# Kernel tuning notes

Measured on AMD Instinct MI355X. Metric: run time of the kernel, lower is better.

The kernel has to match this reference:

```python
import jax, jax.numpy as jnp
import numpy as np

HIDDEN = 4096
NUM_HEADS = 32
NUM_KV_HEADS = 8
HEAD_DIM = HIDDEN // NUM_HEADS  # 128
Q_SIZE = NUM_HEADS * HEAD_DIM    # 4096
KV_SIZE = NUM_KV_HEADS * HEAD_DIM  # 1024
SCALE = 1.0 / HEAD_DIM  # attention_multiplier=None -> head_dim ** (-1)
ROPE_BASE = 10000.0


def _rope_neox(x, positions):
    # x: [B, S, H, D], positions: [B, S] int
    half = HEAD_DIM // 2
    inv_freq = 1.0 / (ROPE_BASE ** (jnp.arange(0, half, dtype=jnp.float32) / half))
    freqs = positions.astype(jnp.float32)[..., None] * inv_freq  # [B, S, half]
    cos = jnp.cos(freqs)[:, :, None, :]  # [B, S, 1, half]
    sin = jnp.sin(freqs)[:, :, None, :]
    x1, x2 = x[..., :half], x[..., half:]
    return jnp.concatenate([x1 * cos - x2 * sin, x2 * cos + x1 * sin], axis=-1)


def setup_inputs() -> dict:
    key = jax.random.key(0)
    k1, k2, k3 = jax.random.split(key, 3)
    B, S = 2, 2048
    positions = jnp.broadcast_to(jnp.arange(S, dtype=jnp.int32), (B, S))
    hidden_states = jax.random.normal(k1, (B, S, HIDDEN), dtype=jnp.float32) * 0.02
    w_qkv = jax.random.normal(k2, (Q_SIZE + 2 * KV_SIZE, HIDDEN), dtype=jnp.float32) * 0.02
    w_o = jax.random.normal(k3, (HIDDEN, Q_SIZE), dtype=jnp.float32) * 0.02
    return {"positions": positions, "hidden_states": hidden_states, "w_qkv": w_qkv, "w_o": w_o}


def reference(positions, hidden_states, w_qkv, w_o):
    B, S, _ = hidden_states.shape
    # fused QKV projection
    qkv = jnp.einsum('bsh,oh->bso', hidden_states, w_qkv)
    q = qkv[..., :Q_SIZE].reshape(B, S, NUM_HEADS, HEAD_DIM)
    k = qkv[..., Q_SIZE:Q_SIZE + KV_SIZE].reshape(B, S, NUM_KV_HEADS, HEAD_DIM)
    v = qkv[..., Q_SIZE + KV_SIZE:].reshape(B, S, NUM_KV_HEADS, HEAD_DIM)
    # neox-style RoPE on q and k
    q = _rope_neox(q, positions)
    k = _rope_neox(k, positions)
    # GQA: repeat kv heads
    rep = NUM_HEADS // NUM_KV_HEADS
    k = jnp.repeat(k, rep, axis=2)  # [B, S, NUM_HEADS, D]
    v = jnp.repeat(v, rep, axis=2)
    # causal attention
    scores = jnp.einsum('bqhd,bkhd->bhqk', q, k) * SCALE
    causal = jnp.tril(jnp.ones((S, S), dtype=bool))
    scores = jnp.where(causal, scores, jnp.finfo(scores.dtype).min)
    probs = jax.nn.softmax(scores, axis=-1)
    attn = jnp.einsum('bhqk,bkhd->bqhd', probs, v).reshape(B, S, Q_SIZE)
    # output projection
    return jnp.einsum('bsq,hq->bsh', attn, w_o)
```

## Files before the change

### kernel.cpp

```cpp
#include <hip/hip_runtime.h>
#include <hip/hip_bf16.h>
#include <cmath>

typedef __bf16 bf16x8 __attribute__((ext_vector_type(8)));
typedef __bf16 bf16x4 __attribute__((ext_vector_type(4)));
typedef float  f32x4  __attribute__((ext_vector_type(4)));
typedef unsigned int u32;
typedef u32 u32x4 __attribute__((ext_vector_type(4)));

#define AS1 __attribute__((address_space(1)))
#define AS3 __attribute__((address_space(3)))
#define GLDS16(gp, lp) __builtin_amdgcn_global_load_lds((AS1 void*)(gp), (AS3 void*)(lp), 16, 0, 0)

#define B_DIM 2
#define S_LEN 2048
#define HIDDEN 4096
#define NHEADS 32
#define NKV 8
#define HDIM 128
#define QSZ 4096
#define KVSZ 1024
#define QKVSZ 6144
#define GK 4096
#define ATT_SCALE 0.0078125f
#define L2E 1.4426950408889634f

__global__ __launch_bounds__(256) void conv_f32_bf16(const float* __restrict__ in,
                                                     __bf16* __restrict__ out, int n4) {
    int idx = blockIdx.x * 256 + threadIdx.x;
    if (idx < n4) {
        float4 v = ((const float4*)in)[idx];
        bf16x4 o;
        o[0] = (__bf16)v.x; o[1] = (__bf16)v.y; o[2] = (__bf16)v.z; o[3] = (__bf16)v.w;
        ((bf16x4*)out)[idx] = o;
    }
}

__global__ __launch_bounds__(256) void rope_table_kernel(float* __restrict__ ct,
                                                         float* __restrict__ st) {
    int idx = blockIdx.x * 256 + threadIdx.x;
    int p = idx >> 6, i = idx & 63;
    float inv = expf(-(float)i * (9.210340371976184f / 64.0f));
    float freq = (float)p * inv;
    float s, c;
    sincosf(freq, &s, &c);
    ct[idx] = c; st[idx] = s;
}

template<typename OUT>
__global__ __launch_bounds__(512, 2) void gemm256(const __bf16* __restrict__ A,
                                                  const __bf16* __restrict__ B,
                                                  OUT* __restrict__ C,
                                                  int N) {
    __shared__ __bf16 Asm[2 * 16384 + 2 * 16384];
    char* Bbase = (char*)Asm + 65536;

    const int tid = threadIdx.x;
    const int w = tid >> 6, l = tid & 63;
    const int l15 = l & 15, l4 = l >> 4;
    const int wr = w >> 2, wc = w & 3;

    const int nwg = gridDim.x * gridDim.y;
    const int orig = blockIdx.y * gridDim.x + blockIdx.x;
    const int swz = (orig & 7) * (nwg >> 3) + (orig >> 3);
    const int bx = swz % gridDim.x, by = swz / gridDim.x;
    const int m0 = by * 256, n0 = bx * 256;

    const __bf16* Ag = A + (size_t)m0 * GK;
    const __bf16* Bg = B + (size_t)n0 * GK;

#define STAGE_AQ(q, tile) do {                                                  \
        int c_ = (q) * 512 + tid;                                               \
        int r_ = c_ >> 3;                                                       \
        int jg_ = (tid & 7) ^ (r_ & 7);                                         \
        GLDS16(Ag + (size_t)r_ * GK + (tile) * 64 + jg_ * 8,                    \
               (char*)Asm + ((tile) & 1) * 32768 + c_ * 16);                    \
    } while (0)
#define STAGE_BS(s, tile) do {                                                  \
        _Pragma("unroll")                                                       \
        for (int i_ = 0; i_ < 2; ++i_) {                                        \
            int v_ = i_ * 512 + tid;                                            \
            int r_ = (v_ >> 8) * 64 + (s) * 32 + ((v_ >> 3) & 31);              \
            int jg_ = (v_ & 7) ^ (r_ & 7);                                      \
            int c_ = r_ * 8 + (v_ & 7);                                         \
            GLDS16(Bg + (size_t)r_ * GK + (tile) * 64 + jg_ * 8,                \
                   Bbase + ((tile) & 1) * 32768 + c_ * 16);                     \
        }                                                                       \
    } while (0)

#define LOAD_A(DST, MH) do {                                                    \
        _Pragma("unroll")                                                       \
        for (int m2 = 0; m2 < 4; ++m2) {                                        \
            int row = wr * 128 + ((MH) * 4 + m2) * 16 + l15;                    \
            _Pragma("unroll")                                                   \
            for (int kk = 0; kk < 2; ++kk) {                                    \
                int j = (kk * 4 + l4) ^ (row & 7);                              \
                DST[m2][kk] = *(const bf16x8*)(Als + row * 64 + j * 8);         \
            }                                                                   \
        }                                                                       \
    } while (0)
#define LOAD_B(DST, NH) do {                                                    \
        _Pragma("unroll")                                                       \
        for (int n2 = 0; n2 < 2; ++n2) {                                        \
            int row = wc * 64 + ((NH) * 2 + n2) * 16 + l15;                     \
            _Pragma("unroll")                                                   \
            for (int kk = 0; kk < 2; ++kk) {                                    \
                int j = (kk * 4 + l4) ^ (row & 7);                              \
                DST[n2][kk] = *(const bf16x8*)(Bls + row * 64 + j * 8);         \
            }                                                                   \
        }                                                                       \
    } while (0)
#define MFMA_QUAD(AF, BF, MI0, NI0)                                             \
    _Pragma("unroll")                                                           \
    for (int m2 = 0; m2 < 4; ++m2)                                              \
        _Pragma("unroll")                                                       \
        for (int n2 = 0; n2 < 2; ++n2)                                          \
            _Pragma("unroll")                                                   \
            for (int kk = 0; kk < 2; ++kk)                                      \
                acc[(MI0) + m2][(NI0) + n2] =                                   \
                    __builtin_amdgcn_mfma_f32_16x16x32_bf16(                    \
                        AF[m2][kk], BF[n2][kk], acc[(MI0) + m2][(NI0) + n2], 0, 0, 0);
#define PH_SYNC_PRE  do { __builtin_amdgcn_sched_barrier(0);                    \
        __builtin_amdgcn_s_barrier();                                           \
        asm volatile("s_waitcnt lgkmcnt(0)" ::: "memory");                      \
        __builtin_amdgcn_sched_barrier(0); } while (0)
#define PH_SYNC_POST do { __builtin_amdgcn_sched_barrier(0);                    \
        __builtin_amdgcn_s_barrier(); } while (0)

    f32x4 acc[8][4] = {};

    const int T = GK / 64;
    STAGE_AQ(0, 0); STAGE_AQ(1, 0); STAGE_AQ(2, 0); STAGE_AQ(3, 0);
    STAGE_BS(0, 0); STAGE_BS(1, 0);
    STAGE_AQ(0, 1); STAGE_AQ(2, 1); STAGE_BS(0, 1);
    asm volatile("s_waitcnt vmcnt(4)" ::: "memory");
    __builtin_amdgcn_s_barrier();

    for (int t = 0; t < T; ++t) {
        const __bf16* Als = Asm + (t & 1) * 16384;
        const __bf16* Bls = (__bf16*)Bbase + (t & 1) * 16384;
        bf16x8 af0[4][2], af1[4][2], bfr[2][2];
        LOAD_A(af0, 0);
        LOAD_B(bfr, 0);
        if (t + 1 < T) { STAGE_AQ(1, t + 1); STAGE_AQ(3, t + 1); }
        PH_SYNC_PRE;
        __builtin_amdgcn_s_setprio(1);
        MFMA_QUAD(af0, bfr, 0, 0);
        __builtin_amdgcn_s_setprio(0);
        PH_SYNC_POST;
        LOAD_B(bfr, 1);
        if (t + 1 < T) STAGE_BS(1, t + 1);
        PH_SYNC_PRE;
        __builtin_amdgcn_s_setprio(1);
        MFMA_QUAD(af0, bfr, 0, 2);
        __builtin_amdgcn_s_setprio(0);
        PH_SYNC_POST;
        LOAD_A(af1, 1);
        LOAD_B(bfr, 0);
        if (t + 2 < T) { STAGE_AQ(0, t + 2); STAGE_AQ(2, t + 2); }
        PH_SYNC_PRE;
        __builtin_amdgcn_s_setprio(1);
        MFMA_QUAD(af1, bfr, 4, 0);
        __builtin_amdgcn_s_setprio(0);
        PH_SYNC_POST;
        LOAD_B(bfr, 1);
        if (t + 2 < T) STAGE_BS(0, t + 2);
        PH_SYNC_PRE;
        __builtin_amdgcn_s_setprio(1);
        MFMA_QUAD(af1, bfr, 4, 2);
        __builtin_amdgcn_s_setprio(0);
        if (t + 2 < T)      { asm volatile("s_waitcnt vmcnt(4)" ::: "memory"); }
        else if (t + 1 < T) { asm volatile("s_waitcnt vmcnt(0)" ::: "memory"); }
        PH_SYNC_POST;
    }
#undef PH_SYNC_PRE
#undef PH_SYNC_POST
#undef MFMA_QUAD
#undef LOAD_A
#undef LOAD_B
#undef STAGE_AQ
#undef STAGE_BS

#pragma unroll
    for (int mi = 0; mi < 8; ++mi)
#pragma unroll
        for (int ni = 0; ni < 4; ++ni)
#pragma unroll
            for (int r = 0; r < 4; ++r)
                C[(size_t)(m0 + wr * 128 + mi * 16 + l4 * 4 + r) * N
                  + n0 + wc * 64 + ni * 16 + l15] = (OUT)acc[mi][ni][r];
}

__global__ __launch_bounds__(256) void rope_kernel(const __bf16* __restrict__ qkv,
                                                   const int* __restrict__ pos,
                                                   const float* __restrict__ ct,
                                                   const float* __restrict__ st,
                                                   __bf16* __restrict__ Qb,
                                                   __bf16* __restrict__ Kb) {
    const int tid = threadIdx.x;
    const int tok = blockIdx.x;
    const int b = tok >> 11, s = tok & 2047;
    const int p = pos[tok];
    const __bf16* base = qkv + (size_t)tok * QKVSZ;
    const float* cb = ct + (size_t)p * 64;
    const float* sb = st + (size_t)p * 64;
    for (int idx = tid; idx < 2560; idx += 256) {
        int head = idx >> 6, i = idx & 63;
        float c = cb[i], sn = sb[i];
        if (head < 32) {
            float x1 = (float)base[head * HDIM + i];
            float x2 = (float)base[head * HDIM + 64 + i];
            size_t o = ((size_t)(b * 32 + head) * S_LEN + s) * HDIM + i;
            Qb[o]      = (__bf16)((x1 * c - x2 * sn) * ATT_SCALE);
            Qb[o + 64] = (__bf16)((x2 * c + x1 * sn) * ATT_SCALE);
        } else {
            int g = head - 32;
            float x1 = (float)base[QSZ + g * HDIM + i];
            float x2 = (float)base[QSZ + g * HDIM + 64 + i];
            size_t o = ((size_t)(b * 8 + g) * S_LEN + s) * HDIM + i;
            Kb[o]      = (__bf16)(x1 * c - x2 * sn);
            Kb[o + 64] = (__bf16)(x2 * c + x1 * sn);
        }
    }
}

__global__ __launch_bounds__(256) void vtrans_kernel(const __bf16* __restrict__ qkv,
                                                     __bf16* __restrict__ Vt) {
    __shared__ __bf16 T[64][132];
    const int tid = threadIdx.x;
    const int st = blockIdx.x, g = blockIdx.y, b = blockIdx.z;
    const __bf16* src = qkv + ((size_t)(b * S_LEN + st * 64)) * QKVSZ + (QSZ + KVSZ) + g * HDIM;
#pragma unroll
    for (int it = 0; it < 8; ++it) {
        int c = it * 256 + tid;
        int row = c >> 5;
        int c4 = c & 31;
        bf16x4 v = *(const bf16x4*)(src + (size_t)row * QKVSZ + c4 * 4);
        *(bf16x4*)(&T[row][c4 * 4]) = v;
    }
    __syncthreads();
#pragma unroll
    for (int it = 0; it < 8; ++it) {
        int c = it * 256 + tid;
        int d = c >> 4;
        int s4 = (c & 15) * 4;
        bf16x4 o;
        o[0] = T[s4 + 0][d]; o[1] = T[s4 + 1][d]; o[2] = T[s4 + 2][d]; o[3] = T[s4 + 3][d];
        *(bf16x4*)(Vt + ((size_t)(b * 8 + g) * HDIM + d) * S_LEN + st * 64 + s4) = o;
    }
}

__global__ __launch_bounds__(512, 2) void attn_kernel(const __bf16* __restrict__ Q,
                                                      const __bf16* __restrict__ K,
                                                      const __bf16* __restrict__ Vt,
                                                      __bf16* __restrict__ O) {
    const int tid = threadIdx.x;
    const int w = tid >> 6, l = tid & 63;
    const int l15 = l & 15, l4 = l >> 4;
    const int flat = blockIdx.x + (blockIdx.y << 2) + (blockIdx.z << 7);
    const int swz = (flat & 7) * 32 + (flat >> 3);
    const int p = swz & 3;
    const int hb = swz >> 2;
    const int h = hb & 31, b = hb >> 5;
    const int g = h >> 2;

    __shared__ __bf16 Ks[4][64 * 128];
    __shared__ __bf16 Vs[4][128 * 64];

    const __bf16* Kp = K + (size_t)(b * 8 + g) * S_LEN * HDIM;
    const __bf16* Vp = Vt + (size_t)(b * 8 + g) * HDIM * S_LEN;

#define RED16(x, OPINS) do {                                                      \
        u32 ra_ = __builtin_bit_cast(u32, x), rb_;                                \
        asm("v_mov_b32 %0, %1" : "=v"(rb_) : "v"(ra_));                           \
        asm("v_permlane16_swap_b32 %0, %1" : "+v"(ra_), "+v"(rb_));               \
        x = OPINS(__builtin_bit_cast(float, ra_), __builtin_bit_cast(float, rb_));\
    } while (0)
#define RED32(x, OPINS) do {                                                      \
        u32 ra_ = __builtin_bit_cast(u32, x), rb_;                                \
        asm("v_mov_b32 %0, %1" : "=v"(rb_) : "v"(ra_));                           \
        asm("v_permlane32_swap_b32 %0, %1" : "+v"(ra_), "+v"(rb_));               \
        x = OPINS(__builtin_bit_cast(float, ra_), __builtin_bit_cast(float, rb_));\
    } while (0)
#define FADD_(a_, b_) ((a_) + (b_))

#define STAGE(ktile) do {                                                          \
        const int buf_ = (ktile) & 3;                                              \
        const __bf16* kbase = Kp + (size_t)(ktile) * 64 * HDIM;                    \
        _Pragma("unroll")                                                          \
        for (int i_ = 0; i_ < 2; ++i_) {                                           \
            int c_ = i_ * 512 + tid;                \
            int row_ = c_ >> 4, cc_ = (c_ & 15) ^ (row_ & 7);                      \
            GLDS16(kbase + (size_t)row_ * HDIM + cc_ * 8,                          \
                   (char*)Ks[buf_] + c_ * 16);                                     \
        }                                                                          \
        const __bf16* vbase = Vp + (size_t)(ktile) * 64;                           \
        _Pragma("unroll")                                                          \
        for (int i_ = 0; i_ < 2; ++i_) {                                           \
            int c_ = i_ * 512 + tid;                \
            int row_ = c_ >> 3, cc_ = (c_ & 7) ^ (row_ & 7);                       \
            GLDS16(vbase + (size_t)row_ * S_LEN + cc_ * 8,                         \
                   (char*)Vs[buf_] + c_ * 16);                                     \
        }                                                                          \
    } while (0)

    for (int pi = 0; pi < 2; ++pi) {
        const int qt = pi ? (7 - p) : p;
        const int qw0 = qt * 256 + w * 32;
        const __bf16* Qp = Q + ((size_t)((b * 32 + h) * S_LEN + qw0)) * HDIM;

        bf16x8 qf[2][4];
#pragma unroll
        for (int qh = 0; qh < 2; ++qh)
#pragma unroll
            for (int kk = 0; kk < 4; ++kk)
                qf[qh][kk] = *(const bf16x8*)(Qp + (size_t)(qh * 16 + l15) * HDIM + kk * 32 + l4 * 8);

        f32x4 acc[2][8] = {};
        float m[2]    = {-1e30f, -1e30f};
        float lsum[2] = {0.f, 0.f};

        const int nkt = 4 * qt + 4;
        if (pi) { asm volatile("s_waitcnt vmcnt(0)" ::: "memory"); }
        STAGE(0);
        STAGE(1);
        STAGE(2);

        for (int kt = 0; kt < nkt; ++kt) {
            if (kt + 3 < nkt) STAGE(kt + 3);
            {
                int rem = nkt - 1 - kt;
                if (rem >= 3)      { asm volatile("s_waitcnt vmcnt(12)" ::: "memory"); }
                else if (rem == 2) { asm volatile("s_waitcnt vmcnt(8)"  ::: "memory"); }
                else if (rem == 1) { asm volatile("s_waitcnt vmcnt(4)"  ::: "memory"); }
                else               { asm volatile("s_waitcnt vmcnt(0)"  ::: "memory"); }
            }
            __builtin_amdgcn_sched_barrier(0);
            __builtin_amdgcn_s_barrier();
            __builtin_amdgcn_sched_barrier(0);
            const int cur = kt & 3;
            if (kt * 64 <= qw0 + 31) {
                f32x4 sfr[2][4];
                __builtin_amdgcn_s_setprio(1);
#pragma unroll
                for (int fn = 0; fn < 4; ++fn) {
                    f32x4 sa0 = {}, sa1 = {};
#pragma unroll
                    for (int kk = 0; kk < 4; ++kk) {
                        int row = fn * 16 + l15;
                        int cc = (kk * 4 + l4) ^ (l15 & 7);
                        bf16x8 kb = *(const bf16x8*)(Ks[cur] + row * HDIM + cc * 8);
                        sa0 = __builtin_amdgcn_mfma_f32_16x16x32_bf16(kb, qf[0][kk], sa0, 0, 0, 0);
                        sa1 = __builtin_amdgcn_mfma_f32_16x16x32_bf16(kb, qf[1][kk], sa1, 0, 0, 0);
                    }
                    sfr[0][fn] = sa0; sfr[1][fn] = sa1;
                }
                __builtin_amdgcn_s_setprio(0);
                const bool needmask = (kt * 64 + 63 > qw0);
                bf16x8 pb[2][2];
#pragma unroll
                for (int qh = 0; qh < 2; ++qh) {
                    const int qrow = qw0 + qh * 16 + l15;
                    float pmax = -1e30f;
#pragma unroll
                    for (int fn = 0; fn < 4; ++fn)
#pragma unroll
                        for (int r = 0; r < 4; ++r) {
                            float v = sfr[qh][fn][r];
                            if (needmask) {
                                int kcol = kt * 64 + fn * 16 + l4 * 4 + r;
                                if (kcol > qrow) v = -1e30f;
                            }
                            sfr[qh][fn][r] = v;
                            pmax = fmaxf(pmax, v);
                        }
                    RED16(pmax, fmaxf);
                    RED32(pmax, fmaxf);
                    if (!__all(pmax - m[qh] <= 8.0f)) {
                        float mn = fmaxf(m[qh], pmax);
                        float alpha = exp2f((m[qh] - mn) * L2E);
                        m[qh] = mn;
                        lsum[qh] *= alpha;
#pragma unroll
                        for (int n = 0; n < 8; ++n)
#pragma unroll
                            for (int r = 0; r < 4; ++r) acc[qh][n][r] *= alpha;
                    }
                    float rs = 0.f;
                    u32 pk01[4], pk23[4];
#pragma unroll
                    for (int fn = 0; fn < 4; ++fn) {
                        float p0 = exp2f((sfr[qh][fn][0] - m[qh]) * L2E);
                        float p1 = exp2f((sfr[qh][fn][1] - m[qh]) * L2E);
                        float p2 = exp2f((sfr[qh][fn][2] - m[qh]) * L2E);
                        float p3 = exp2f((sfr[qh][fn][3] - m[qh]) * L2E);
                        rs += (p0 + p1) + (p2 + p3);
                        asm("v_cvt_pk_bf16_f32 %0, %1, %2" : "=v"(pk01[fn]) : "v"(p0), "v"(p1));
                        asm("v_cvt_pk_bf16_f32 %0, %1, %2" : "=v"(pk23[fn]) : "v"(p2), "v"(p3));
                    }
                    RED16(rs, FADD_);
                    RED32(rs, FADD_);
                    lsum[qh] += rs;
#pragma unroll
                    for (int kk = 0; kk < 2; ++kk) {
                        u32 w0 = pk01[2 * kk], w2 = pk01[2 * kk + 1];
                        asm("v_permlane32_swap_b32 %0, %1" : "+v"(w0), "+v"(w2));
                        asm("v_permlane16_swap_b32 %0, %1" : "+v"(w0), "+v"(w2));
                        u32 w1 = pk23[2 * kk], w3 = pk23[2 * kk + 1];
                        asm("v_permlane32_swap_b32 %0, %1" : "+v"(w1), "+v"(w3));
                        asm("v_permlane16_swap_b32 %0, %1" : "+v"(w1), "+v"(w3));
                        u32x4 wv;
                        wv[0] = w0; wv[1] = w1; wv[2] = w2; wv[3] = w3;
                        pb[qh][kk] = __builtin_bit_cast(bf16x8, wv);
                    }
                }
                __builtin_amdgcn_s_setprio(1);
#pragma unroll
                for (int kk = 0; kk < 2; ++kk) {
#pragma unroll
                    for (int n = 0; n < 8; ++n) {
                        int row = n * 16 + l15;
                        int cc = (kk * 4 + l4) ^ (l15 & 7);
                        bf16x8 vb = *(const bf16x8*)(Vs[cur] + row * 64 + cc * 8);
                        acc[0][n] = __builtin_amdgcn_mfma_f32_16x16x32_bf16(vb, pb[0][kk], acc[0][n], 0, 0, 0);
                        acc[1][n] = __builtin_amdgcn_mfma_f32_16x16x32_bf16(vb, pb[1][kk], acc[1][n], 0, 0, 0);
                    }
                }
                __builtin_amdgcn_s_setprio(0);
            }
            __builtin_amdgcn_sched_barrier(0);
            __builtin_amdgcn_s_barrier();
            __builtin_amdgcn_sched_barrier(0);
        }
#pragma unroll
        for (int qh = 0; qh < 2; ++qh) {
            float inv = 1.0f / lsum[qh];
            int qrow = qw0 + qh * 16 + l15;
            __bf16* obase = O + ((size_t)(b * S_LEN) + qrow) * QSZ + h * HDIM + l4 * 4;
#pragma unroll
            for (int n = 0; n < 8; ++n) {
                bf16x4 o4;
#pragma unroll
                for (int r = 0; r < 4; ++r) o4[r] = (__bf16)(acc[qh][n][r] * inv);
                *(bf16x4*)(obase + n * 16) = o4;
            }
        }
    }
#undef STAGE
#undef RED16
#undef RED32
#undef FADD_
}

extern "C" void kernel_launch(void* const* d_in, const int* in_sizes, int n_in,
                              void* d_out, int out_size, void* d_ws, size_t ws_size,
                              hipStream_t stream) {
    const int*   pos    = (const int*)d_in[0];
    const float* hidden = (const float*)d_in[1];
    const float* wqkv   = (const float*)d_in[2];
    const float* wo     = (const float*)d_in[3];
    float* out = (float*)d_out;

    __bf16* hb    = (__bf16*)d_ws;
    __bf16* wqb   = hb  + 16777216;
    __bf16* wob   = wqb + 25165824;
    __bf16* qkv   = wob + 16777216;
    __bf16* Qb    = qkv + 25165824;
    __bf16* Kb    = Qb  + 16777216;
    __bf16* Vtb   = Kb  + 4194304;
    __bf16* attnb = Vtb + 4194304;
    float*  rc    = (float*)(attnb + 16777216);
    float*  rs    = rc + 131072;

    conv_f32_bf16<<<16384, 256, 0, stream>>>(hidden, hb, 4194304);
    conv_f32_bf16<<<24576, 256, 0, stream>>>(wqkv, wqb, 6291456);
    conv_f32_bf16<<<16384, 256, 0, stream>>>(wo, wob, 4194304);
    rope_table_kernel<<<512, 256, 0, stream>>>(rc, rs);
    gemm256<__bf16><<<dim3(QKVSZ / 256, (B_DIM * S_LEN) / 256), 512, 0, stream>>>(hb, wqb, qkv, QKVSZ);
    rope_kernel<<<B_DIM * S_LEN, 256, 0, stream>>>(qkv, pos, rc, rs, Qb, Kb);
    vtrans_kernel<<<dim3(S_LEN / 64, NKV, B_DIM), 256, 0, stream>>>(qkv, Vtb);
    attn_kernel<<<dim3(4, NHEADS, B_DIM), 512, 0, stream>>>(Qb, Kb, Vtb, attnb);
    gemm256<float><<<dim3(HIDDEN / 256, (B_DIM * S_LEN) / 256), 512, 0, stream>>>(attnb, wob, out, HIDDEN);
}
```

Before: 531.1 us.

## Restructure GEMM mainloop into 4-stage K=32 pipeline with one barrier per tile

Replaces the double-buffered K=64 GEMM mainloop, which had four phases each split by paired barriers, with a four-stage ring of K=32 tiles. Three tiles are prefetched ahead, and each iteration has a single vmcnt wait plus one barrier. All A and B fragments are loaded before running 32 MFMAs per tile. This cuts barrier count and sync overhead per K step and deepens global-to-LDS prefetch, at the cost of less interleaving between LDS reads and MFMAs within a tile, and a narrower 4-chunk XOR swizzle that may raise LDS bank conflicts.

```diff
diff --git a/kernel.cpp b/kernel.cpp
--- a/kernel.cpp
+++ b/kernel.cpp
@@ -52,8 +52,8 @@
                                                   const __bf16* __restrict__ B,
                                                   OUT* __restrict__ C,
                                                   int N) {
-    __shared__ __bf16 Asm[2 * 16384 + 2 * 16384];
-    char* Bbase = (char*)Asm + 65536;
+    __shared__ __bf16 Asm[4 * 8192];
+    __shared__ __bf16 Bsm[4 * 8192];
 
     const int tid = threadIdx.x;
     const int w = tid >> 6, l = tid & 63;
@@ -69,117 +69,74 @@
     const __bf16* Ag = A + (size_t)m0 * GK;
     const __bf16* Bg = B + (size_t)n0 * GK;
 
-#define STAGE_AQ(q, tile) do {                                                  \
-        int c_ = (q) * 512 + tid;                                               \
-        int r_ = c_ >> 3;                                                       \
-        int jg_ = (tid & 7) ^ (r_ & 7);                                         \
-        GLDS16(Ag + (size_t)r_ * GK + (tile) * 64 + jg_ * 8,                    \
-               (char*)Asm + ((tile) & 1) * 32768 + c_ * 16);                    \
-    } while (0)
-#define STAGE_BS(s, tile) do {                                                  \
+#define STAGE(tile) do {                                                        \
+        const int s_ = (tile) & 3;                                              \
         _Pragma("unroll")                                                       \
         for (int i_ = 0; i_ < 2; ++i_) {                                        \
-            int v_ = i_ * 512 + tid;                                            \
-            int r_ = (v_ >> 8) * 64 + (s) * 32 + ((v_ >> 3) & 31);              \
-            int jg_ = (v_ & 7) ^ (r_ & 7);                                      \
-            int c_ = r_ * 8 + (v_ & 7);                                         \
-            GLDS16(Bg + (size_t)r_ * GK + (tile) * 64 + jg_ * 8,                \
-                   Bbase + ((tile) & 1) * 32768 + c_ * 16);                     \
+            int c_ = i_ * 512 + tid;                  \
+            int r_ = c_ >> 2;                                                   \
+            int jg_ = (c_ & 3) ^ (r_ & 3);                                      \
+            GLDS16(Ag + (size_t)r_ * GK + (tile) * 32 + jg_ * 8,                \
+                   (char*)Asm + s_ * 16384 + c_ * 16);                          \
+            GLDS16(Bg + (size_t)r_ * GK + (tile) * 32 + jg_ * 8,                \
+                   (char*)Bsm + s_ * 16384 + c_ * 16);                          \
         }                                                                       \
     } while (0)
 
-#define LOAD_A(DST, MH) do {                                                    \
-        _Pragma("unroll")                                                       \
-        for (int m2 = 0; m2 < 4; ++m2) {                                        \
-            int row = wr * 128 + ((MH) * 4 + m2) * 16 + l15;                    \
-            _Pragma("unroll")                                                   \
-            for (int kk = 0; kk < 2; ++kk) {                                    \
-                int j = (kk * 4 + l4) ^ (row & 7);                              \
-                DST[m2][kk] = *(const bf16x8*)(Als + row * 64 + j * 8);         \
-            }                                                                   \
-        }                                                                       \
-    } while (0)
-#define LOAD_B(DST, NH) do {                                                    \
-        _Pragma("unroll")                                                       \
-        for (int n2 = 0; n2 < 2; ++n2) {                                        \
-            int row = wc * 64 + ((NH) * 2 + n2) * 16 + l15;                     \
-            _Pragma("unroll")                                                   \
-            for (int kk = 0; kk < 2; ++kk) {                                    \
-                int j = (kk * 4 + l4) ^ (row & 7);                              \
-                DST[n2][kk] = *(const bf16x8*)(Bls + row * 64 + j * 8);         \
-            }                                                                   \
-        }                                                                       \
-    } while (0)
-#define MFMA_QUAD(AF, BF, MI0, NI0)                                             \
-    _Pragma("unroll")                                                           \
-    for (int m2 = 0; m2 < 4; ++m2)                                              \
-        _Pragma("unroll")                                                       \
-        for (int n2 = 0; n2 < 2; ++n2)                                          \
-            _Pragma("unroll")                                                   \
-            for (int kk = 0; kk < 2; ++kk)                                      \
-                acc[(MI0) + m2][(NI0) + n2] =                                   \
-                    __builtin_amdgcn_mfma_f32_16x16x32_bf16(                    \
-                        AF[m2][kk], BF[n2][kk], acc[(MI0) + m2][(NI0) + n2], 0, 0, 0);
-#define PH_SYNC_PRE  do { __builtin_amdgcn_sched_barrier(0);                    \
-        __builtin_amdgcn_s_barrier();                                           \
-        asm volatile("s_waitcnt lgkmcnt(0)" ::: "memory");                      \
-        __builtin_amdgcn_sched_barrier(0); } while (0)
-#define PH_SYNC_POST do { __builtin_amdgcn_sched_barrier(0);                    \
-        __builtin_amdgcn_s_barrier(); } while (0)
-
     f32x4 acc[8][4] = {};
 
-    const int T = GK / 64;
-    STAGE_AQ(0, 0); STAGE_AQ(1, 0); STAGE_AQ(2, 0); STAGE_AQ(3, 0);
-    STAGE_BS(0, 0); STAGE_BS(1, 0);
-    STAGE_AQ(0, 1); STAGE_AQ(2, 1); STAGE_BS(0, 1);
-    asm volatile("s_waitcnt vmcnt(4)" ::: "memory");
-    __builtin_amdgcn_s_barrier();
+    const int T = GK / 32;
+    STAGE(0); STAGE(1); STAGE(2);
 
     for (int t = 0; t < T; ++t) {
-        const __bf16* Als = Asm + (t & 1) * 16384;
-        const __bf16* Bls = (__bf16*)Bbase + (t & 1) * 16384;
-        bf16x8 af0[4][2], af1[4][2], bfr[2][2];
-        LOAD_A(af0, 0);
-        LOAD_B(bfr, 0);
-        if (t + 1 < T) { STAGE_AQ(1, t + 1); STAGE_AQ(3, t + 1); }
-        PH_SYNC_PRE;
+        {
+            int rem = T - 1 - t;
+            if (rem >= 2)      { asm volatile("s_waitcnt vmcnt(8)" ::: "memory"); }
+            else if (rem == 1) { asm volatile("s_waitcnt vmcnt(4)" ::: "memory"); }
+            else               { asm volatile("s_waitcnt vmcnt(0)" ::: "memory"); }
+        }
+        __builtin_amdgcn_sched_barrier(0);
+        __builtin_amdgcn_s_barrier();
+        __builtin_amdgcn_sched_barrier(0);
+        if (t + 3 < T) STAGE(t + 3);
+
+        const __bf16* Als = Asm + (t & 3) * 8192;
+        const __bf16* Bls = Bsm + (t & 3) * 8192;
+        bf16x8 af0[4], af1[4], bfr[4];
+#pragma unroll
+        for (int m2 = 0; m2 < 4; ++m2) {
+            int row = wr * 128 + m2 * 16 + l15;
+            int j = l4 ^ (row & 3);
+            af0[m2] = *(const bf16x8*)(Als + row * 32 + j * 8);
+        }
+#pragma unroll
+        for (int n2 = 0; n2 < 4; ++n2) {
+            int row = wc * 64 + n2 * 16 + l15;
+            int j = l4 ^ (row & 3);
+            bfr[n2] = *(const bf16x8*)(Bls + row * 32 + j * 8);
+        }
+#pragma unroll
+        for (int m2 = 0; m2 < 4; ++m2) {
+            int row = wr * 128 + (4 + m2) * 16 + l15;
+            int j = l4 ^ (row & 3);
+            af1[m2] = *(const bf16x8*)(Als + row * 32 + j * 8);
+        }
         __builtin_amdgcn_s_setprio(1);
-        MFMA_QUAD(af0, bfr, 0, 0);
+#pragma unroll
+        for (int m2 = 0; m2 < 4; ++m2)
+#pragma unroll
+            for (int n2 = 0; n2 < 4; ++n2)
+                acc[m2][n2] = __builtin_amdgcn_mfma_f32_16x16x32_bf16(
+                    af0[m2], bfr[n2], acc[m2][n2], 0, 0, 0);
+#pragma unroll
+        for (int m2 = 0; m2 < 4; ++m2)
+#pragma unroll
+            for (int n2 = 0; n2 < 4; ++n2)
+                acc[4 + m2][n2] = __builtin_amdgcn_mfma_f32_16x16x32_bf16(
+                    af1[m2], bfr[n2], acc[4 + m2][n2], 0, 0, 0);
         __builtin_amdgcn_s_setprio(0);
-        PH_SYNC_POST;
-        LOAD_B(bfr, 1);
-        if (t + 1 < T) STAGE_BS(1, t + 1);
-        PH_SYNC_PRE;
-        __builtin_amdgcn_s_setprio(1);
-        MFMA_QUAD(af0, bfr, 0, 2);
-        __builtin_amdgcn_s_setprio(0);
-        PH_SYNC_POST;
-        LOAD_A(af1, 1);
-        LOAD_B(bfr, 0);
-        if (t + 2 < T) { STAGE_AQ(0, t + 2); STAGE_AQ(2, t + 2); }
-        PH_SYNC_PRE;
-        __builtin_amdgcn_s_setprio(1);
-        MFMA_QUAD(af1, bfr, 4, 0);
-        __builtin_amdgcn_s_setprio(0);
-        PH_SYNC_POST;
-        LOAD_B(bfr, 1);
-        if (t + 2 < T) STAGE_BS(0, t + 2);
-        PH_SYNC_PRE;
-        __builtin_amdgcn_s_setprio(1);
-        MFMA_QUAD(af1, bfr, 4, 2);
-        __builtin_amdgcn_s_setprio(0);
-        if (t + 2 < T)      { asm volatile("s_waitcnt vmcnt(4)" ::: "memory"); }
-        else if (t + 1 < T) { asm volatile("s_waitcnt vmcnt(0)" ::: "memory"); }
-        PH_SYNC_POST;
-    }
-#undef PH_SYNC_PRE
-#undef PH_SYNC_POST
-#undef MFMA_QUAD
-#undef LOAD_A
-#undef LOAD_B
-#undef STAGE_AQ
-#undef STAGE_BS
+    }
+#undef STAGE
 
 #pragma unroll
     for (int mi = 0; mi < 8; ++mi)
```

New measurement: 732.3 us. +37.9%, slower.
